# Kernel tuning notes

Hardware: AMD Instinct MI355X
Metric: run time of the kernel (lower is better)

## Reference

```python
import jax, jax.numpy as jnp
import numpy as np

NUM_STEPS = 5
RELAX = 1.5
EPS = 1e-5
SIZE = 128
OUT = 128
HSIZE = SIZE + OUT  # feature transformer width (256)


def bn_inf(x, g, b, m, v):
    # inference batch norm with running stats
    return g * (x - m) * jax.lax.rsqrt(v + EPS) + b


def glu(h):
    return h[:, :HSIZE] * jax.nn.sigmoid(h[:, HSIZE:])


def sparsemax(z):
    d = z.shape[-1]
    z_sorted = -jnp.sort(-z, axis=-1)  # descending
    z_cum = jnp.cumsum(z_sorted, axis=-1)
    k = jnp.arange(1, d + 1, dtype=z.dtype)
    support = 1.0 + k * z_sorted > z_cum
    k_z = jnp.sum(support, axis=-1, keepdims=True)  # int support size
    tau = (jnp.take_along_axis(z_cum, k_z - 1, axis=-1) - 1.0) / k_z.astype(z.dtype)
    return jnp.maximum(z - tau, 0.0)


def feat_transformer(x, Ws0, Ws1, Wu_t, g, b, m, v):
    # 4 GLU FeatureBlocks: blocks 0,1 use shared fc weights, 2,3 unshared
    sqrt_half = jnp.sqrt(jnp.asarray(0.5, x.dtype))
    h = glu(bn_inf(x @ Ws0, g[0], b[0], m[0], v[0]))
    h = h * sqrt_half + glu(bn_inf(h @ Ws1, g[1], b[1], m[1], v[1]))
    h = h * sqrt_half + glu(bn_inf(h @ Wu_t[0], g[2], b[2], m[2], v[2]))
    h = h * sqrt_half + glu(bn_inf(h @ Wu_t[1], g[3], b[3], m[3], v[3]))
    return h


def setup_inputs() -> dict:
    key = jax.random.key(0)
    ks = jax.random.split(key, 20)
    B, F = 32768, 512
    U = 2 * HSIZE  # GLU fc units = 512
    T = NUM_STEPS + 1
    sc = 0.05
    inp = {}
    inp['features'] = jax.random.normal(ks[0], (B, F), jnp.float32)
    inp['bn0_g'] = 1.0 + 0.1 * jax.random.normal(ks[1], (F,), jnp.float32)
    inp['bn0_b'] = 0.1 * jax.random.normal(ks[2], (F,), jnp.float32)
    inp['bn0_m'] = 0.1 * jax.random.normal(ks[3], (F,), jnp.float32)
    inp['bn0_v'] = jax.random.uniform(ks[4], (F,), jnp.float32, 0.5, 1.5)
    inp['Ws0'] = sc * jax.random.normal(ks[5], (F, U), jnp.float32)
    inp['Ws1'] = sc * jax.random.normal(ks[6], (HSIZE, U), jnp.float32)
    inp['Wu'] = sc * jax.random.normal(ks[7], (T, 2, HSIZE, U), jnp.float32)
    inp['ft_g'] = 1.0 + 0.1 * jax.random.normal(ks[8], (T, 4, U), jnp.float32)
    inp['ft_b'] = 0.1 * jax.random.normal(ks[9], (T, 4, U), jnp.float32)
    inp['ft_m'] = 0.1 * jax.random.normal(ks[10], (T, 4, U), jnp.float32)
    inp['ft_v'] = jax.random.uniform(ks[11], (T, 4, U), jnp.float32, 0.5, 1.5)
    inp['W_att'] = sc * jax.random.normal(ks[12], (NUM_STEPS, SIZE, F), jnp.float32)
    inp['att_g'] = 1.0 + 0.1 * jax.random.normal(ks[13], (NUM_STEPS, F), jnp.float32)
    inp['att_b'] = 0.1 * jax.random.normal(ks[14], (NUM_STEPS, F), jnp.float32)
    inp['att_m'] = 0.1 * jax.random.normal(ks[15], (NUM_STEPS, F), jnp.float32)
    inp['att_v'] = jax.random.uniform(ks[16], (NUM_STEPS, F), jnp.float32, 0.5, 1.5)
    inp['Wf'] = sc * jax.random.normal(ks[17], (SIZE, OUT), jnp.float32)
    inp['bf'] = jnp.zeros((OUT,), jnp.float32)
    return inp


def reference(features, bn0_g, bn0_b, bn0_m, bn0_v, Ws0, Ws1, Wu,
              ft_g, ft_b, ft_m, ft_v, W_att, att_g, att_b, att_m, att_v, Wf, bf):
    B = features.shape[0]
    feats = bn_inf(features, bn0_g, bn0_b, bn0_m, bn0_v)
    prior = jnp.ones_like(feats)
    out_acc = jnp.zeros((B, OUT), feats.dtype)
    x = feat_transformer(feats, Ws0, Ws1, Wu[0], ft_g[0], ft_b[0], ft_m[0], ft_v[0])
    masks = []
    for s in range(NUM_STEPS):
        att = bn_inf(x[:, OUT:] @ W_att[s], att_g[s], att_b[s], att_m[s], att_v[s])
        mask = sparsemax(att * prior)
        prior = prior * (RELAX - mask)
        masks.append(mask)
        x = feat_transformer(mask * feats, Ws0, Ws1, Wu[s + 1],
                             ft_g[s + 1], ft_b[s + 1], ft_m[s + 1], ft_v[s + 1])
        out_acc = out_acc + jax.nn.relu(x[:, :OUT])
    final = out_acc @ Wf + bf
    return final, jnp.stack(masks)
```

## Files before the change

### kernel.cpp

```cpp
#include <hip/hip_runtime.h>
#include <hip/hip_bf16.h>
#include <math.h>

#define B_ROWS   32768
#define NSTEPS   5
#define EPS_BN   1e-5f
#define RELAX_C  1.5f
#define SQRT_HALF 0.70710678118654752440f

typedef _Float16 f16;
typedef _Float16 f16x4 __attribute__((ext_vector_type(4)));
typedef _Float16 f16x8 __attribute__((ext_vector_type(8)));
typedef float    f32x4 __attribute__((ext_vector_type(4)));

__device__ __forceinline__ int glu_perm2(int c) {
    int g = c >> 5, o = c & 31;
    return (o < 16) ? (g * 16 + o) : (g * 16 + (o - 16) + 256);
}

__device__ __forceinline__ void gload16(const void* g, void* l) {
    __builtin_amdgcn_global_load_lds(
        (const __attribute__((address_space(1))) unsigned int*)g,
        (__attribute__((address_space(3))) unsigned int*)l, 16, 0, 0);
}

__global__ void prep_all(
    const float* __restrict__ bn0_g, const float* __restrict__ bn0_b,
    const float* __restrict__ bn0_m, const float* __restrict__ bn0_v,
    const float* __restrict__ ft_g, const float* __restrict__ ft_b,
    const float* __restrict__ ft_m, const float* __restrict__ ft_v,
    const float* __restrict__ att_g, const float* __restrict__ att_b,
    const float* __restrict__ att_m, const float* __restrict__ att_v,
    const float* __restrict__ Ws0, const float* __restrict__ Ws1,
    const float* __restrict__ Wu,  const float* __restrict__ Wat,
    const float* __restrict__ features,
    float* __restrict__ ftS, float* __restrict__ ftH,
    float* __restrict__ attS, float* __restrict__ attH,
    f16* __restrict__ ws0, f16* __restrict__ ws1,
    f16* __restrict__ wu,  f16* __restrict__ wat,
    f16* __restrict__ feats, float* __restrict__ oacc)
{
    const int blk = blockIdx.x;
    if (blk < 60) {
        int idx = blk * 256 + threadIdx.x;
        if (idx < 24 * 512) {
            int tb = idx >> 9;
            int c = idx & 511;
            int src = tb * 512 + glu_perm2(c);
            float s = ft_g[src] * rsqrtf(ft_v[src] + EPS_BN);
            ftS[idx] = s;
            ftH[idx] = ft_b[src] - ft_m[src] * s;
        } else if (idx < 24 * 512 + 5 * 512) {
            int q = idx - 24 * 512;
            float s = att_g[q] * rsqrtf(att_v[q] + EPS_BN);
            attS[q] = s;
            attH[q] = att_b[q] - att_m[q] * s;
        }
    } else if (blk < 9020) {
        int i = (blk - 60) * 256 + threadIdx.x;
        if (i < 262144) {
            int n = i >> 9, k = i & 511;
            ws0[i] = (f16)Ws0[(k << 9) + glu_perm2(n)];
        } else if (i < 393216) {
            int j = i - 262144;
            int n = j >> 8, k = j & 255;
            ws1[j] = (f16)Ws1[(k << 9) + glu_perm2(n)];
        } else if (i < 1966080) {
            int j = i - 393216;
            int mat = j >> 17;
            int r = j & 131071;
            int n = r >> 8, k = r & 255;
            wu[j] = (f16)Wu[(mat << 17) + (k << 9) + glu_perm2(n)];
        } else if (i < 2293760) {
            int j = i - 1966080;
            int mat = j >> 16;
            int r = j & 65535;
            int n = r >> 7, k = r & 127;
            wat[j] = (f16)Wat[(mat << 16) + (k << 9) + n];
        }
    } else {
        const int b = blk - 9020;
        if (b < 16384) {
            int i = b * 256 + threadIdx.x;
            int base = i * 4;
            int c = base & 511;
            float4 xv = *(const float4*)(features + base);
            f16x4 hv;
            float s0 = bn0_g[c]     * rsqrtf(bn0_v[c]     + EPS_BN);
            float s1 = bn0_g[c + 1] * rsqrtf(bn0_v[c + 1] + EPS_BN);
            float s2 = bn0_g[c + 2] * rsqrtf(bn0_v[c + 2] + EPS_BN);
            float s3 = bn0_g[c + 3] * rsqrtf(bn0_v[c + 3] + EPS_BN);
            hv.x = (f16)((xv.x - bn0_m[c])     * s0 + bn0_b[c]);
            hv.y = (f16)((xv.y - bn0_m[c + 1]) * s1 + bn0_b[c + 1]);
            hv.z = (f16)((xv.z - bn0_m[c + 2]) * s2 + bn0_b[c + 2]);
            hv.w = (f16)((xv.w - bn0_m[c + 3]) * s3 + bn0_b[c + 3]);
            *(f16x4*)(feats + base) = hv;
        } else {
            int i = (b - 16384) * 256 + threadIdx.x;
            ((float4*)oacc)[i] = make_float4(0.f, 0.f, 0.f, 0.f);
        }
    }
}

template<int MODE, int NT>
__global__ __launch_bounds__(512, 4) void gemm_conveyor(
    const f16* __restrict__ A, const int ldA,
    const f16* __restrict__ B,
    const float* __restrict__ scale, const float* __restrict__ shift,
    const f16* __restrict__ res,
    f16* __restrict__ out,
    float* __restrict__ oacc)
{
    constexpr int K = NT * 32;
    __shared__ __align__(16) char smem[3 * 24576];
    const int tid  = threadIdx.x;
    const int lane = tid & 63;
    const int w    = tid >> 6;
    const int wm   = w >> 1;
    const int wn   = w & 1;
    const int lr   = lane & 15;
    const int lh   = lane >> 4;
    const int d    = blockIdx.x;
    const int bid  = (d & 7) * 64 + (d >> 3);
    const int row0 = (bid >> 2) * 256;
    const int bcol = (bid & 3) * 128;

    const int c0 = 3 * w, c1 = 3 * w + 1, c2 = 3 * w + 2;
    const bool a0 = c0 < 16, a1 = c1 < 16, a2 = c2 < 16;
    const char* p0 = a0 ? (const char*)(A + (size_t)(row0 + c0 * 16 + lr) * ldA + lh * 8)
                        : (const char*)(B + (size_t)(bcol + (c0 - 16) * 16 + lr) * K + lh * 8);
    const char* p1 = a1 ? (const char*)(A + (size_t)(row0 + c1 * 16 + lr) * ldA + lh * 8)
                        : (const char*)(B + (size_t)(bcol + (c1 - 16) * 16 + lr) * K + lh * 8);
    const char* p2 = a2 ? (const char*)(A + (size_t)(row0 + c2 * 16 + lr) * ldA + lh * 8)
                        : (const char*)(B + (size_t)(bcol + (c2 - 16) * 16 + lr) * K + lh * 8);
    const int d0 = c0 * 1024, d1 = c1 * 1024, d2 = c2 * 1024;

    f32x4 acc[4][4];
    #pragma unroll
    for (int m = 0; m < 4; ++m)
        #pragma unroll
        for (int n = 0; n < 4; ++n)
            acc[m][n] = f32x4{0.f, 0.f, 0.f, 0.f};

    auto STAGE = [&](int s) {
        const int ko = s * 64;
        char* ring = smem + (s % 3) * 24576;
        gload16(p0 + ko, ring + d0);
        gload16(p1 + ko, ring + d1);
        gload16(p2 + ko, ring + d2);
    };

    STAGE(0); STAGE(1);

    for (int s = 0; s < NT; ++s) {
        if (s + 1 < NT) asm volatile("s_waitcnt vmcnt(3)" ::: "memory");
        else            asm volatile("s_waitcnt vmcnt(0)" ::: "memory");
        __builtin_amdgcn_s_barrier();
        asm volatile("" ::: "memory");
        if (s + 2 < NT) STAGE(s + 2);

        const char* L = smem + (s % 3) * 24576;
        f16x8 a[4], b[4];
        #pragma unroll
        for (int m = 0; m < 4; ++m)
            a[m] = *(const f16x8*)(L + (wm * 4 + m) * 1024 + lane * 16);
        #pragma unroll
        for (int n = 0; n < 4; ++n)
            b[n] = *(const f16x8*)(L + 16384 + (wn * 4 + n) * 1024 + lane * 16);
        __builtin_amdgcn_s_setprio(1);
        #pragma unroll
        for (int n = 0; n < 4; ++n)
            #pragma unroll
            for (int m = 0; m < 4; ++m)
                acc[m][n] = __builtin_amdgcn_mfma_f32_16x16x32_f16(a[m], b[n], acc[m][n], 0, 0, 0);
        __builtin_amdgcn_s_setprio(0);
    }

    const int rbase = row0 + wm * 64;
    #pragma unroll
    for (int p = 0; p < 2; ++p) {
        const int cb = bcol + wn * 64 + p * 32;
        const float sA = scale[cb + lr],      hA = shift[cb + lr];
        const float sB = scale[cb + 16 + lr], hB = shift[cb + 16 + lr];
        const int oc = (cb >> 1) + lr;
        #pragma unroll
        for (int m = 0; m < 4; ++m) {
            #pragma unroll
            for (int r = 0; r < 4; ++r) {
                const int row = rbase + m * 16 + lh * 4 + r;
                float y0 = acc[m][2 * p][r]     * sA + hA;
                float y1 = acc[m][2 * p + 1][r] * sB + hB;
                float val = y0 / (1.f + expf(-y1));
                if constexpr (MODE >= 1)
                    val += SQRT_HALF * (float)res[(size_t)row * 256 + oc];
                if constexpr (MODE <= 1) {
                    out[(size_t)row * 256 + oc] = (f16)val;
                } else {
                    if (oc < 128) {
                        if (oacc) oacc[(size_t)row * 128 + oc] += fmaxf(val, 0.f);
                    } else {
                        out[(size_t)row * 128 + (oc - 128)] = (f16)val;
                    }
                }
            }
        }
    }
}

template<int USE_PRIOR>
__global__ __launch_bounds__(512, 4) void att_sparsemax_kernel(
    const f16* __restrict__ A,
    const f16* __restrict__ Bw,
    const float* __restrict__ scale, const float* __restrict__ shift,
    const f16* __restrict__ feats,
    f16* __restrict__ prior,
    float* __restrict__ mask_out,
    f16* __restrict__ mf)
{
    __shared__ f16 attLds[64 * 512];
    const int tid  = threadIdx.x;
    const int lane = tid & 63;
    const int w    = tid >> 6;
    const int dd   = blockIdx.x;
    const int bid  = (dd & 7) * 64 + (dd >> 3);
    const int brow = bid * 64;
    const int lr   = lane & 15;
    const int lk   = (lane >> 4) * 8;

    f32x4 acc[4][4];
    #pragma unroll
    for (int m = 0; m < 4; ++m)
        #pragma unroll
        for (int n = 0; n < 4; ++n)
            acc[m][n] = f32x4{0.f, 0.f, 0.f, 0.f};

    const f16* pa = A + (size_t)(brow + lr) * 128 + lk;
    const f16* pb = Bw + (size_t)(w * 64 + lr) * 128 + lk;

    #pragma unroll
    for (int t = 0; t < 4; ++t) {
        f16x8 a[4], b[4];
        #pragma unroll
        for (int m = 0; m < 4; ++m) a[m] = *(const f16x8*)(pa + m * 16 * 128 + t * 32);
        #pragma unroll
        for (int n = 0; n < 4; ++n) b[n] = *(const f16x8*)(pb + n * 16 * 128 + t * 32);
        __builtin_amdgcn_s_setprio(1);
        #pragma unroll
        for (int n = 0; n < 4; ++n)
            #pragma unroll
            for (int m = 0; m < 4; ++m)
                acc[m][n] = __builtin_amdgcn_mfma_f32_16x16x32_f16(a[m], b[n], acc[m][n], 0, 0, 0);
        __builtin_amdgcn_s_setprio(0);
    }

    #pragma unroll
    for (int n = 0; n < 4; ++n) {
        const int col = w * 64 + n * 16 + lr;
        const float s = scale[col], h = shift[col];
        #pragma unroll
        for (int m = 0; m < 4; ++m) {
            const int r0 = m * 16 + (lane >> 4) * 4;
            #pragma unroll
            for (int r = 0; r < 4; ++r)
                attLds[(r0 + r) * 512 + col] = (f16)(acc[m][n][r] * s + h);
        }
    }
    __syncthreads();

    const int cb8 = lane * 8;
    for (int rr = 0; rr < 8; ++rr) {
        const int row = w * 8 + rr;
        const int grow = brow + row;
        const size_t g8 = (size_t)grow * 512 + cb8;

        float z[8], pr[8];
        f16x8 prv;
        if (USE_PRIOR) prv = *(const f16x8*)(prior + g8);
        f16x8 zv = *(const f16x8*)(&attLds[row * 512 + cb8]);
        #pragma unroll
        for (int j = 0; j < 8; ++j) {
            pr[j] = USE_PRIOR ? (float)prv[j] : 1.0f;
            z[j] = (float)zv[j] * pr[j];
        }
        float mx = z[0];
        #pragma unroll
        for (int j = 1; j < 8; ++j) mx = fmaxf(mx, z[j]);
        #pragma unroll
        for (int off = 32; off; off >>= 1) mx = fmaxf(mx, __shfl_xor(mx, off));

        float tau = mx - 1.0f;
        for (int it = 0; it < 20; ++it) {
            float s = 0.f, c = 0.f;
            #pragma unroll
            for (int j = 0; j < 8; ++j) {
                float dz = z[j] - tau;
                if (dz > 0.f) { s += dz; c += 1.f; }
            }
            #pragma unroll
            for (int off = 32; off; off >>= 1) {
                s += __shfl_xor(s, off);
                c += __shfl_xor(c, off);
            }
            float tn = tau + (s - 1.0f) / c;
            if (!(tn > tau)) break;
            tau = tn;
        }

        float mk[8];
        f16x8 pnew, mfv;
        f16x8 fv = *(const f16x8*)(feats + g8);
        #pragma unroll
        for (int j = 0; j < 8; ++j) {
            mk[j] = fmaxf(z[j] - tau, 0.f);
            pnew[j] = (f16)(pr[j] * (RELAX_C - mk[j]));
            mfv[j] = (f16)(mk[j] * (float)fv[j]);
        }
        f32x4 m0 = {mk[0], mk[1], mk[2], mk[3]};
        f32x4 m1 = {mk[4], mk[5], mk[6], mk[7]};
        __builtin_nontemporal_store(m0, (f32x4*)(mask_out + g8));
        __builtin_nontemporal_store(m1, (f32x4*)(mask_out + g8 + 4));
        *(f16x8*)(prior + g8) = pnew;
        *(f16x8*)(mf + g8) = mfv;
    }
}

__global__ __launch_bounds__(256) void gemm_f32_final(
    const float* __restrict__ A,
    const float* __restrict__ W,
    const float* __restrict__ bias,
    float* __restrict__ out)
{
    __shared__ float As[16][128];
    __shared__ float Bs[16][128];
    const int tid = threadIdx.x;
    const int tm = tid >> 4, tn = tid & 15;
    const int brow = blockIdx.x * 128;
    float acc[8][8] = {};
    for (int k0 = 0; k0 < 128; k0 += 16) {
        #pragma unroll
        for (int i = 0; i < 2; ++i) {
            int f = tid + i * 256;
            int row = f >> 2, kq = (f & 3) << 2;
            float4 av = *(const float4*)(A + (size_t)(brow + row) * 128 + k0 + kq);
            As[kq + 0][row] = av.x;
            As[kq + 1][row] = av.y;
            As[kq + 2][row] = av.z;
            As[kq + 3][row] = av.w;
            int kr = f >> 5, nq = (f & 31) << 2;
            *(float4*)(&Bs[kr][nq]) = *(const float4*)(W + (size_t)(k0 + kr) * 128 + nq);
        }
        __syncthreads();
        #pragma unroll
        for (int kk = 0; kk < 16; ++kk) {
            float a[8], b[8];
            *(float4*)(a)     = *(const float4*)(&As[kk][tm * 8]);
            *(float4*)(a + 4) = *(const float4*)(&As[kk][tm * 8 + 4]);
            *(float4*)(b)     = *(const float4*)(&Bs[kk][tn * 8]);
            *(float4*)(b + 4) = *(const float4*)(&Bs[kk][tn * 8 + 4]);
            #pragma unroll
            for (int i = 0; i < 8; ++i)
                #pragma unroll
                for (int j = 0; j < 8; ++j)
                    acc[i][j] += a[i] * b[j];
        }
        __syncthreads();
    }
    #pragma unroll
    for (int i = 0; i < 8; ++i) {
        int row = brow + tm * 8 + i;
        #pragma unroll
        for (int j = 0; j < 8; ++j)
            out[(size_t)row * 128 + tn * 8 + j] = acc[i][j] + bias[tn * 8 + j];
    }
}

extern "C" void kernel_launch(void* const* d_in, const int* in_sizes, int n_in,
                              void* d_out, int out_size, void* d_ws, size_t ws_size,
                              hipStream_t stream)
{
    const float* features = (const float*)d_in[0];
    const float* bn0_g = (const float*)d_in[1];
    const float* bn0_b = (const float*)d_in[2];
    const float* bn0_m = (const float*)d_in[3];
    const float* bn0_v = (const float*)d_in[4];
    const float* Ws0   = (const float*)d_in[5];
    const float* Ws1   = (const float*)d_in[6];
    const float* Wu    = (const float*)d_in[7];
    const float* ft_g  = (const float*)d_in[8];
    const float* ft_b  = (const float*)d_in[9];
    const float* ft_m  = (const float*)d_in[10];
    const float* ft_v  = (const float*)d_in[11];
    const float* W_att = (const float*)d_in[12];
    const float* att_g = (const float*)d_in[13];
    const float* att_b = (const float*)d_in[14];
    const float* att_m = (const float*)d_in[15];
    const float* att_v = (const float*)d_in[16];
    const float* Wf    = (const float*)d_in[17];
    const float* bf    = (const float*)d_in[18];
    float* out = (float*)d_out;

    char* wp = (char*)d_ws;
    auto alloc = [&](size_t bytes) { char* r = wp; wp += (bytes + 255) & ~(size_t)255; return r; };
    const size_t BR = B_ROWS;
    f16* feats  = (f16*)alloc(BR * 512 * 2);
    f16* mfbuf  = (f16*)alloc(BR * 512 * 2);
    f16* ubuf   = (f16*)alloc(BR * 256 * 2);
    f16* vbuf   = (f16*)alloc(BR * 256 * 2);
    f16* xhalf  = (f16*)alloc(BR * 128 * 2);
    f16* prior  = (f16*)alloc(BR * 512 * 2);
    float* oacc  = (float*)alloc(BR * 128 * 4);
    f16* ws0  = (f16*)alloc(512 * 512 * 2);
    f16* ws1  = (f16*)alloc(512 * 256 * 2);
    f16* wu   = (f16*)alloc((size_t)12 * 512 * 256 * 2);
    f16* wat  = (f16*)alloc((size_t)5 * 512 * 128 * 2);
    float* ftS  = (float*)alloc(24 * 512 * 4);
    float* ftH  = (float*)alloc(24 * 512 * 4);
    float* attS = (float*)alloc(5 * 512 * 4);
    float* attH = (float*)alloc(5 * 512 * 4);

    prep_all<<<29500, 256, 0, stream>>>(
        bn0_g, bn0_b, bn0_m, bn0_v, ft_g, ft_b, ft_m, ft_v,
        att_g, att_b, att_m, att_v, Ws0, Ws1, Wu, W_att, features,
        ftS, ftH, attS, attH, ws0, ws1, wu, wat, feats, oacc);

    auto ft = [&](const f16* in, int t, bool accum) {
        const f16* wu0 = wu + (size_t)(t * 2 + 0) * 131072;
        const f16* wu1 = wu + (size_t)(t * 2 + 1) * 131072;
        gemm_conveyor<0, 16><<<512, 512, 0, stream>>>(in, 512, ws0,
            ftS + (t * 4 + 0) * 512, ftH + (t * 4 + 0) * 512,
            nullptr, ubuf, nullptr);
        gemm_conveyor<1, 8><<<512, 512, 0, stream>>>(ubuf, 256, ws1,
            ftS + (t * 4 + 1) * 512, ftH + (t * 4 + 1) * 512,
            ubuf, vbuf, nullptr);
        gemm_conveyor<1, 8><<<512, 512, 0, stream>>>(vbuf, 256, wu0,
            ftS + (t * 4 + 2) * 512, ftH + (t * 4 + 2) * 512,
            vbuf, ubuf, nullptr);
        gemm_conveyor<2, 8><<<512, 512, 0, stream>>>(ubuf, 256, wu1,
            ftS + (t * 4 + 3) * 512, ftH + (t * 4 + 3) * 512,
            ubuf, xhalf, accum ? oacc : nullptr);
    };

    ft(feats, 0, false);

    for (int s = 0; s < NSTEPS; ++s) {
        float* mask_s = out + 4194304 + (size_t)s * 16777216;
        if (s == 0)
            att_sparsemax_kernel<0><<<512, 512, 0, stream>>>(
                xhalf, wat + (size_t)s * 65536,
                attS + s * 512, attH + s * 512,
                feats, prior, mask_s, mfbuf);
        else
            att_sparsemax_kernel<1><<<512, 512, 0, stream>>>(
                xhalf, wat + (size_t)s * 65536,
                attS + s * 512, attH + s * 512,
                feats, prior, mask_s, mfbuf);
        ft(mfbuf, s + 1, true);
    }

    gemm_f32_final<<<B_ROWS / 128, 256, 0, stream>>>(oacc, Wf, bf, out);
}
```

Baseline: 934.7 us.

## Fuse all GEMM and sparsemax stages into one persistent kernel with per-gang barriers

Replaces the 29 separate GEMM and attention/sparsemax launches with a single persistent kernel. Each group of four blocks shares a 256-row slab and synchronises through a per-gang atomic counter barrier instead of kernel boundaries. This removes launch gaps and full-device drains, so gangs can run ahead of one another. In exchange, template specialisation becomes runtime branches (mode, NT, use_prior), which may cost registers and unrolling, and correctness relies on all 512 blocks being co-resident to avoid deadlock.

Result: slower. 2.469 ms (+164.2%).

```diff
diff --git a/kernel.cpp b/kernel.cpp
--- a/kernel.cpp
+++ b/kernel.cpp
@@ -38,7 +38,8 @@
     float* __restrict__ attS, float* __restrict__ attH,
     f16* __restrict__ ws0, f16* __restrict__ ws1,
     f16* __restrict__ wu,  f16* __restrict__ wat,
-    f16* __restrict__ feats, float* __restrict__ oacc)
+    f16* __restrict__ feats, float* __restrict__ oacc,
+    unsigned int* __restrict__ gcnt)
 {
     const int blk = blockIdx.x;
     if (blk < 60) {
@@ -78,7 +79,7 @@
             int n = r >> 7, k = r & 127;
             wat[j] = (f16)Wat[(mat << 16) + (k << 9) + n];
         }
-    } else {
+    } else if (blk < 29500) {
         const int b = blk - 9020;
         if (b < 16384) {
             int i = b * 256 + threadIdx.x;
@@ -99,20 +100,33 @@
             int i = (b - 16384) * 256 + threadIdx.x;
             ((float4*)oacc)[i] = make_float4(0.f, 0.f, 0.f, 0.f);
         }
-    }
-}
-
-template<int MODE, int NT>
-__global__ __launch_bounds__(512, 4) void gemm_conveyor(
-    const f16* __restrict__ A, const int ldA,
+    } else {
+        if (threadIdx.x < 128) gcnt[threadIdx.x] = 0u;
+    }
+}
+
+__device__ __forceinline__ void gbar(unsigned int* cnt, unsigned int tgt) {
+    __syncthreads();
+    if (threadIdx.x == 0) {
+        __threadfence();
+        atomicAdd(cnt, 1u);
+        while (atomicAdd(cnt, 0u) < tgt)
+            __builtin_amdgcn_s_sleep(8);
+        __threadfence();
+    }
+    __syncthreads();
+}
+
+__device__ __forceinline__ void gemm_stage(
+    char* __restrict__ smem,
+    const f16* __restrict__ A, const int ldA, const int NT,
     const f16* __restrict__ B,
     const float* __restrict__ scale, const float* __restrict__ shift,
     const f16* __restrict__ res,
-    f16* __restrict__ out,
-    float* __restrict__ oacc)
-{
-    constexpr int K = NT * 32;
-    __shared__ __align__(16) char smem[3 * 24576];
+    f16* __restrict__ outp, float* __restrict__ oa,
+    const int mode, const int row0, const int bcol)
+{
+    const int K    = NT * 32;
     const int tid  = threadIdx.x;
     const int lane = tid & 63;
     const int w    = tid >> 6;
@@ -120,10 +134,6 @@
     const int wn   = w & 1;
     const int lr   = lane & 15;
     const int lh   = lane >> 4;
-    const int d    = blockIdx.x;
-    const int bid  = (d & 7) * 64 + (d >> 3);
-    const int row0 = (bid >> 2) * 256;
-    const int bcol = (bid & 3) * 128;
 
     const int c0 = 3 * w, c1 = 3 * w + 1, c2 = 3 * w + 2;
     const bool a0 = c0 < 16, a1 = c1 < 16, a2 = c2 < 16;
@@ -191,15 +201,15 @@
                 float y0 = acc[m][2 * p][r]     * sA + hA;
                 float y1 = acc[m][2 * p + 1][r] * sB + hB;
                 float val = y0 / (1.f + expf(-y1));
-                if constexpr (MODE >= 1)
+                if (mode >= 1)
                     val += SQRT_HALF * (float)res[(size_t)row * 256 + oc];
-                if constexpr (MODE <= 1) {
-                    out[(size_t)row * 256 + oc] = (f16)val;
+                if (mode <= 1) {
+                    outp[(size_t)row * 256 + oc] = (f16)val;
                 } else {
                     if (oc < 128) {
-                        if (oacc) oacc[(size_t)row * 128 + oc] += fmaxf(val, 0.f);
+                        if (oa) oa[(size_t)row * 128 + oc] += fmaxf(val, 0.f);
                     } else {
-                        out[(size_t)row * 128 + (oc - 128)] = (f16)val;
+                        outp[(size_t)row * 128 + (oc - 128)] = (f16)val;
                     }
                 }
             }
@@ -207,23 +217,21 @@
     }
 }
 
-template<int USE_PRIOR>
-__global__ __launch_bounds__(512, 4) void att_sparsemax_kernel(
+__device__ __forceinline__ void att_stage(
+    char* __restrict__ smem,
     const f16* __restrict__ A,
     const f16* __restrict__ Bw,
     const float* __restrict__ scale, const float* __restrict__ shift,
     const f16* __restrict__ feats,
     f16* __restrict__ prior,
     float* __restrict__ mask_out,
-    f16* __restrict__ mf)
-{
-    __shared__ f16 attLds[64 * 512];
+    f16* __restrict__ mf,
+    const int brow, const int use_prior)
+{
+    f16* attLds = (f16*)smem;
     const int tid  = threadIdx.x;
     const int lane = tid & 63;
     const int w    = tid >> 6;
-    const int dd   = blockIdx.x;
-    const int bid  = (dd & 7) * 64 + (dd >> 3);
-    const int brow = bid * 64;
     const int lr   = lane & 15;
     const int lk   = (lane >> 4) * 8;
 
@@ -253,6 +261,7 @@
         __builtin_amdgcn_s_setprio(0);
     }
 
+    __syncthreads();
     #pragma unroll
     for (int n = 0; n < 4; ++n) {
         const int col = w * 64 + n * 16 + lr;
@@ -275,11 +284,11 @@
 
         float z[8], pr[8];
         f16x8 prv;
-        if (USE_PRIOR) prv = *(const f16x8*)(prior + g8);
+        if (use_prior) prv = *(const f16x8*)(prior + g8);
         f16x8 zv = *(const f16x8*)(&attLds[row * 512 + cb8]);
         #pragma unroll
         for (int j = 0; j < 8; ++j) {
-            pr[j] = USE_PRIOR ? (float)prv[j] : 1.0f;
+            pr[j] = use_prior ? (float)prv[j] : 1.0f;
             z[j] = (float)zv[j] * pr[j];
         }
         float mx = z[0];
@@ -321,6 +330,53 @@
         __builtin_nontemporal_store(m1, (f32x4*)(mask_out + g8 + 4));
         *(f16x8*)(prior + g8) = pnew;
         *(f16x8*)(mf + g8) = mfv;
+    }
+}
+
+__global__ __launch_bounds__(512, 4) void tabnet_persist(
+    const f16* __restrict__ feats, f16* __restrict__ mf,
+    f16* __restrict__ ub, f16* __restrict__ vb,
+    f16* __restrict__ xh, f16* __restrict__ prior, float* __restrict__ oacc,
+    const f16* __restrict__ ws0, const f16* __restrict__ ws1,
+    const f16* __restrict__ wu,  const f16* __restrict__ wat,
+    const float* __restrict__ ftS, const float* __restrict__ ftH,
+    const float* __restrict__ attS, const float* __restrict__ attH,
+    float* __restrict__ out, unsigned int* __restrict__ gcnt)
+{
+    __shared__ __align__(16) char smem[3 * 24576];
+    const int d    = blockIdx.x;
+    const int bid  = (d & 7) * 64 + (d >> 3);
+    const int gang = bid >> 2;
+    const int j    = bid & 3;
+    const int row0 = gang * 256;
+    const int bcol = j * 128;
+    unsigned int* cnt = gcnt + gang;
+    unsigned int ep = 0;
+
+    for (int t = 0; t < 6; ++t) {
+        const f16* in0 = (t == 0) ? feats : mf;
+        #pragma unroll 1
+        for (int g = 0; g < 4; ++g) {
+            const f16* Ag  = (g == 0) ? in0 : ((g == 2) ? vb : ub);
+            const int ldA  = (g == 0) ? 512 : 256;
+            const int NT   = (g == 0) ? 16 : 8;
+            const f16* Bw  = (g == 0) ? ws0 : (g == 1) ? ws1
+                            : wu + (size_t)(t * 2 + (g - 2)) * 131072;
+            f16* outp      = (g == 1) ? vb : ((g == 3) ? xh : ub);
+            const int mode = (g == 0) ? 0 : ((g == 3) ? 2 : 1);
+            float* oa      = (g == 3 && t > 0) ? oacc : nullptr;
+            gemm_stage(smem, Ag, ldA, NT, Bw,
+                       ftS + (t * 4 + g) * 512, ftH + (t * 4 + g) * 512,
+                       Ag, outp, oa, mode, row0, bcol);
+            gbar(cnt, 4u * ++ep);
+        }
+        if (t < 5) {
+            att_stage(smem, xh, wat + (size_t)t * 65536,
+                      attS + t * 512, attH + t * 512,
+                      feats, prior, out + 4194304 + (size_t)t * 16777216, mf,
+                      row0 + j * 64, t != 0);
+            gbar(cnt, 4u * ++ep);
+        }
     }
 }
 
@@ -417,45 +473,16 @@
     float* ftH  = (float*)alloc(24 * 512 * 4);
     float* attS = (float*)alloc(5 * 512 * 4);
     float* attH = (float*)alloc(5 * 512 * 4);
-
-    prep_all<<<29500, 256, 0, stream>>>(
+    unsigned int* gcnt = (unsigned int*)alloc(128 * 4);
+
+    prep_all<<<29501, 256, 0, stream>>>(
         bn0_g, bn0_b, bn0_m, bn0_v, ft_g, ft_b, ft_m, ft_v,
         att_g, att_b, att_m, att_v, Ws0, Ws1, Wu, W_att, features,
-        ftS, ftH, attS, attH, ws0, ws1, wu, wat, feats, oacc);
-
-    auto ft = [&](const f16* in, int t, bool accum) {
-        const f16* wu0 = wu + (size_t)(t * 2 + 0) * 131072;
-        const f16* wu1 = wu + (size_t)(t * 2 + 1) * 131072;
-        gemm_conveyor<0, 16><<<512, 512, 0, stream>>>(in, 512, ws0,
-            ftS + (t * 4 + 0) * 512, ftH + (t * 4 + 0) * 512,
-            nullptr, ubuf, nullptr);
-        gemm_conveyor<1, 8><<<512, 512, 0, stream>>>(ubuf, 256, ws1,
-            ftS + (t * 4 + 1) * 512, ftH + (t * 4 + 1) * 512,
-            ubuf, vbuf, nullptr);
-        gemm_conveyor<1, 8><<<512, 512, 0, stream>>>(vbuf, 256, wu0,
-            ftS + (t * 4 + 2) * 512, ftH + (t * 4 + 2) * 512,
-            vbuf, ubuf, nullptr);
-        gemm_conveyor<2, 8><<<512, 512, 0, stream>>>(ubuf, 256, wu1,
-            ftS + (t * 4 + 3) * 512, ftH + (t * 4 + 3) * 512,
-            ubuf, xhalf, accum ? oacc : nullptr);
-    };
-
-    ft(feats, 0, false);
-
-    for (int s = 0; s < NSTEPS; ++s) {
-        float* mask_s = out + 4194304 + (size_t)s * 16777216;
-        if (s == 0)
-            att_sparsemax_kernel<0><<<512, 512, 0, stream>>>(
-                xhalf, wat + (size_t)s * 65536,
-                attS + s * 512, attH + s * 512,
-                feats, prior, mask_s, mfbuf);
-        else
-            att_sparsemax_kernel<1><<<512, 512, 0, stream>>>(
-                xhalf, wat + (size_t)s * 65536,
-                attS + s * 512, attH + s * 512,
-                feats, prior, mask_s, mfbuf);
-        ft(mfbuf, s + 1, true);
-    }
+        ftS, ftH, attS, attH, ws0, ws1, wu, wat, feats, oacc, gcnt);
+
+    tabnet_persist<<<512, 512, 0, stream>>>(
+        feats, mfbuf, ubuf, vbuf, xhalf, prior, oacc,
+        ws0, ws1, wu, wat, ftS, ftH, attS, attH, out, gcnt);
 
     gemm_f32_final<<<B_ROWS / 128, 256, 0, stream>>>(oacc, Wf, bf, out);
 }
```
